# Kernel optimization log

Hardware: AMD Instinct MI355X
Metric: run time of the kernel (lower is better)

## Reference

```python
import jax, jax.numpy as jnp
import numpy as np

DIM = 512
HEADS = 8
AGENT = 49
POOL = 7  # int(sqrt(49))
EPS = 1e-5  # BatchNorm eps


def _adaptive_avg_pool(x, out_hw):
    # torch AdaptiveAvgPool2d semantics: bin i covers [floor(i*H/out), ceil((i+1)*H/out))
    B, C, H, W = x.shape
    cs = jnp.cumsum(jnp.cumsum(x, axis=2), axis=3)
    cs = jnp.pad(cs, ((0, 0), (0, 0), (1, 0), (1, 0)))  # integral image, [B,C,H+1,W+1]
    hs = np.floor(np.arange(out_hw) * H / out_hw).astype(np.int32)
    he = np.ceil((np.arange(out_hw) + 1) * H / out_hw).astype(np.int32)
    ws = np.floor(np.arange(out_hw) * W / out_hw).astype(np.int32)
    we = np.ceil((np.arange(out_hw) + 1) * W / out_hw).astype(np.int32)
    area = ((he - hs)[:, None] * (we - ws)[None, :]).astype(np.float32)
    s = (cs[:, :, he][:, :, :, we] - cs[:, :, hs][:, :, :, we]
         - cs[:, :, he][:, :, :, ws] + cs[:, :, hs][:, :, :, ws])
    return s / area


def setup_inputs() -> dict:
    key = jax.random.key(0)
    ks = jax.random.split(key, 8)
    d = DIM

    def w(k, shape, s=0.02):
        return jax.random.normal(k, shape, jnp.float32) * s

    return {
        "x": jax.random.normal(ks[0], (16, d, 32, 32), jnp.float32),
        "H": 32,
        "W": 32,
        "q_w": w(ks[1], (d, d)),
        "kv_w": w(ks[2], (2 * d, d)),
        "dw_w": w(ks[3], (d, 1, 3, 3), 0.1),   # depthwise 3x3, groups=d
        "dw_b": jnp.zeros((d,), jnp.float32),
        "bn_gamma": jnp.ones((d,), jnp.float32),
        "bn_beta": jnp.zeros((d,), jnp.float32),
        "bn_mean": jnp.zeros((d,), jnp.float32),
        "bn_var": jnp.ones((d,), jnp.float32),
        "pw_w": w(ks[4], (d, d, 1, 1)),          # pointwise 1x1 conv
        "pw_b": jnp.zeros((d,), jnp.float32),
        "proj_w": w(ks[5], (d, d)),
        "proj_b": jnp.zeros((d,), jnp.float32),
        "enh1_w": w(ks[6], (d, d)),
        "enh1_b": jnp.zeros((d,), jnp.float32),
        "enh2_w": w(ks[7], (d, d)),
        "enh2_b": jnp.zeros((d,), jnp.float32),
    }


def reference(x, H, W, q_w, kv_w, dw_w, dw_b, bn_gamma, bn_beta, bn_mean, bn_var,
              pw_w, pw_b, proj_w, proj_b, enh1_w, enh1_b, enh2_w, enh2_b):
    B, C, H, W = x.shape  # torch re-reads sizes from x
    N = H * W
    hd = C // HEADS
    scale = hd ** -0.5
    dn = ('NCHW', 'OIHW', 'NCHW')

    x_flat = x.reshape(B, C, N).transpose(0, 2, 1)            # [B,N,C]
    q = (x_flat @ q_w.T).reshape(B, N, HEADS, hd).transpose(0, 2, 1, 3)  # [B,h,N,hd]
    kv = (x_flat @ kv_w.T).reshape(B, N, 2, HEADS, hd).transpose(2, 0, 3, 1, 4)
    k, v = kv[0], kv[1]                                        # [B,h,N,hd]

    # agent tokens (faithful raw reshapes as in the torch code)
    a = _adaptive_avg_pool(x, POOL)                            # [B,C,7,7]
    a = a.reshape(B, C, AGENT).transpose(0, 2, 1)              # [B,49,C]
    a = a.reshape(B, C, POOL, POOL)                            # raw reshape (torch bug, kept)
    a = jax.lax.conv_general_dilated(a, dw_w, (1, 1), 'SAME',
                                     feature_group_count=C, dimension_numbers=dn)
    a = a + dw_b[None, :, None, None]
    a = (a - bn_mean[None, :, None, None]) * jax.lax.rsqrt(bn_var + EPS)[None, :, None, None]
    a = a * bn_gamma[None, :, None, None] + bn_beta[None, :, None, None]
    a = jax.nn.relu(a)
    a = jax.lax.conv_general_dilated(a, pw_w, (1, 1), 'SAME', dimension_numbers=dn)
    a = a + pw_b[None, :, None, None]
    a = a.reshape(B, AGENT, C)                                 # raw reshape
    a = a.reshape(B, HEADS, AGENT, hd)                         # raw reshape (torch bug, kept)

    # stage 1: agent <- kv
    agent_attn = jax.nn.softmax(jnp.einsum('bhad,bhnd->bhan', a, k) * scale, axis=-1)
    agg = jnp.einsum('bhan,bhnd->bhad', agent_attn, v)         # [B,h,49,hd]
    # stage 2: q <- agent
    q_attn = jax.nn.softmax(jnp.einsum('bhnd,bhad->bhna', q, a) * scale, axis=-1)
    enh = jnp.einsum('bhna,bhad->bhnd', q_attn, agg)           # [B,h,N,hd]
    enh = enh.transpose(0, 2, 1, 3).reshape(B, N, C)

    x_out = enh @ proj_w.T + proj_b
    out = (jax.nn.relu(x_out @ enh1_w.T + enh1_b) @ enh2_w.T + enh2_b) + x_out
    return out.reshape(B, C, H, W)  # raw reshape as in torch
```

## Files before the change

kernel.cpp:

```cpp
#include <hip/hip_runtime.h>
#include <stdint.h>


typedef float f32x4 __attribute__((ext_vector_type(4)));
typedef short s16x8 __attribute__((ext_vector_type(8)));

typedef __attribute__((address_space(1))) void glob_v;
typedef __attribute__((address_space(3))) void lds_v;
#define GLD16(g, l) \
  __builtin_amdgcn_global_load_lds((glob_v*)(g), (lds_v*)(l), 16, 0, 0)

__device__ __forceinline__ float bf2f(unsigned short u) {
  union { unsigned int i; float f; } v; v.i = ((unsigned int)u) << 16; return v.f;
}
__device__ __forceinline__ unsigned short f2bf(float f) {
  union { float f; unsigned int i; } v; v.f = f;
  return (unsigned short)((v.i + 0x7FFFu + ((v.i >> 16) & 1u)) >> 16);
}

__constant__ int ws7[7] = {0, 4, 9, 13, 18, 22, 27};
__constant__ int we7[7] = {5, 10, 14, 19, 23, 28, 32};

__global__ __launch_bounds__(256) void k_transpose(const float* __restrict__ x,
                                                   unsigned short* __restrict__ xT,
                                                   float* __restrict__ p_rows) {
  __shared__ float tile[64][65];
  const int b = blockIdx.z, c0 = blockIdx.y * 64, n0 = blockIdx.x * 64;
  const int t = threadIdx.x, tn = t & 63, tg = t >> 6;
#pragma unroll
  for (int i = 0; i < 16; ++i) {
    const int c_l = tg * 16 + i;
    tile[c_l][tn] = x[(b * 512 + c0 + c_l) * 1024 + n0 + tn];
  }
  __syncthreads();
#pragma unroll
  for (int i = 0; i < 16; ++i) {
    const int n_l = tg * 16 + i;
    xT[(b * 1024 + n0 + n_l) * 512 + c0 + tn] = f2bf(tile[tn][n_l]);
  }
  if (t < 128) {
    const int c_l = t >> 1, rw = t & 1;
    const int rowg = blockIdx.x * 2 + rw;
    const float* src = &tile[c_l][rw * 32];
    float* dst = p_rows + ((b * 512 + c0 + c_l) * 32 + rowg) * 8;
#pragma unroll
    for (int jb = 0; jb < 7; ++jb) {
      float s = 0.f;
      for (int cc = ws7[jb]; cc < we7[jb]; ++cc) s += src[cc];
      dst[jb] = s;
    }
  }
}

__global__ __launch_bounds__(256) void k_poolred(const float* __restrict__ p_rows,
                                                 float* __restrict__ p) {
  const int u = blockIdx.x * 256 + threadIdx.x;
  if (u >= 401408) return;
  const int bc = u / 49, ij = u % 49;
  const int i = ij / 7, j = ij % 7;
  float s = 0.f;
  for (int r = ws7[i]; r < we7[i]; ++r) s += p_rows[bc * 256 + r * 8 + j];
  const float area = (float)((we7[i] - ws7[i]) * (we7[j] - ws7[j]));
  p[u] = s / area;
}

__global__ __launch_bounds__(256) void k_weights(
    const float* __restrict__ qw, const float* __restrict__ kvw,
    const float* __restrict__ pjw, const float* __restrict__ w1,
    const float* __restrict__ w2, unsigned short* __restrict__ Wqkv,
    unsigned short* __restrict__ Wpj, unsigned short* __restrict__ W1,
    unsigned short* __restrict__ W2) {
  const int u = blockIdx.x * 256 + threadIdx.x;
  const float* s; unsigned short* d; int su, du;
  if (u < 196608) { d = Wqkv; du = u;
    if (u < 65536) { s = qw; su = u; } else { s = kvw; su = u - 65536; } }
  else if (u < 262144) { s = pjw; su = u - 196608; d = Wpj; du = su; }
  else if (u < 327680) { s = w1; su = u - 262144; d = W1; du = su; }
  else { s = w2; su = u - 327680; d = W2; du = su; }
  const f32x4 val = ((const f32x4*)s)[su];
  uint2 pk;
  pk.x = (unsigned)f2bf(val[0]) | ((unsigned)f2bf(val[1]) << 16);
  pk.y = (unsigned)f2bf(val[2]) | ((unsigned)f2bf(val[3]) << 16);
  ((uint2*)d)[du] = pk;
}

__global__ __launch_bounds__(256) void k_dw(
    const float* __restrict__ p, const float* __restrict__ dww,
    const float* __restrict__ dwb, const float* __restrict__ g,
    const float* __restrict__ be, const float* __restrict__ mean,
    const float* __restrict__ var, float* __restrict__ r) {
  const int t = threadIdx.x, s = t & 63;
  if (s >= 49) return;
  const int bc = blockIdx.x * 4 + (t >> 6);
  const int b = bc >> 9, c = bc & 511;
  const int i = s / 7, j = s % 7;
  float sum = 0.f;
#pragma unroll
  for (int ki = 0; ki < 3; ++ki)
#pragma unroll
    for (int kj = 0; kj < 3; ++kj) {
      const int ii = i + ki - 1, jj = j + kj - 1;
      if (ii < 0 || ii > 6 || jj < 0 || jj > 6) continue;
      const int f = c * 49 + ii * 7 + jj;
      sum += dww[c * 9 + ki * 3 + kj] * p[(b * 512 + (f & 511)) * 49 + (f >> 9)];
    }
  sum += dwb[c];
  sum = (sum - mean[c]) * rsqrtf(var[c] + 1e-5f) * g[c] + be[c];
  r[bc * 49 + s] = fmaxf(sum, 0.f);
}

__global__ __launch_bounds__(256) void k_pw(const float* __restrict__ r,
                                            const float* __restrict__ w,
                                            const float* __restrict__ bias,
                                            float* __restrict__ A) {
  __shared__ float wl[128 * 36];
  __shared__ float rl[128 * 64];
  const int blk = blockIdx.x;
  const int b = blk >> 4, cg = blk & 15;
  const int t = threadIdx.x, wv = t >> 6, lane = t & 63;
  float acc[8];
#pragma unroll
  for (int j = 0; j < 8; ++j) acc[j] = 0.f;
  for (int ch = 0; ch < 4; ++ch) {
    __syncthreads();
#pragma unroll
    for (int u = t; u < 4096; u += 256) {
      const int co = u >> 7, ci = u & 127;
      wl[ci * 36 + co] = w[(cg * 32 + co) * 512 + ch * 128 + ci];
    }
    for (int u = t; u < 6272; u += 256) {
      const int ci = u / 49, s = u % 49;
      rl[ci * 64 + s] = r[b * 25088 + ch * 6272 + u];
    }
    __syncthreads();
#pragma unroll 4
    for (int ci = 0; ci < 128; ++ci) {
      const f32x4 w0 = *(const f32x4*)(wl + ci * 36 + wv * 8);
      const f32x4 w1 = *(const f32x4*)(wl + ci * 36 + wv * 8 + 4);
      const float rv = rl[ci * 64 + lane];
#pragma unroll
      for (int j = 0; j < 4; ++j) { acc[j] += w0[j] * rv; acc[4 + j] += w1[j] * rv; }
    }
  }
  if (lane < 49) {
#pragma unroll
    for (int j = 0; j < 8; ++j) {
      const int co = cg * 32 + wv * 8 + j;
      A[b * 25088 + co * 49 + lane] = acc[j] + bias[co];
    }
  }
}

template <int MODE>
__global__ __launch_bounds__(256) void k_gemm(
    const unsigned short* __restrict__ A, const unsigned short* __restrict__ B,
    unsigned short* __restrict__ oq, unsigned short* __restrict__ ok,
    unsigned short* __restrict__ ov, float* __restrict__ of,
    unsigned short* __restrict__ obf, const float* __restrict__ bias,
    const float* __restrict__ resid, float* __restrict__ dout) {
  __shared__ unsigned short As[2][4096];
  __shared__ unsigned short Bs[2][4096];
  const int t = threadIdx.x;
  constexpr int NB = (MODE == 0) ? 12 : 4;
  constexpr int NWG = NB * 128;
  const int swz = ((int)blockIdx.x & 7) * (NWG >> 3) + ((int)blockIdx.x >> 3);
  const int n0 = (swz % NB) * 128, m0 = (swz / NB) * 128;
  const int w = t >> 6, lane = t & 63;
  const int wr = w >> 1, wc = w & 1, lr = lane & 15, lg = lane >> 4;
  const int row = t >> 2, q = t & 3;
  const unsigned short* gA = A + m0 * 512;
  const unsigned short* gB = B + n0 * 512;

  auto stage = [&](int cur, int kt) {
    const unsigned short* sa = gA + row * 512 + kt * 32 + q * 8;
    const unsigned short* sb = gB + row * 512 + kt * 32 + q * 8;
    unsigned short* da = As[cur] + w * 512;
    unsigned short* db = Bs[cur] + w * 512;
    GLD16(sa, da);
    GLD16(sa + 32768, da + 2048);
    GLD16(sb, db);
    GLD16(sb + 32768, db + 2048);
  };

  f32x4 acc[4][4];
#pragma unroll
  for (int mi = 0; mi < 4; ++mi)
#pragma unroll
    for (int ni = 0; ni < 4; ++ni)
#pragma unroll
      for (int rr = 0; rr < 4; ++rr) acc[mi][ni][rr] = 0.f;

  stage(0, 0);
  __syncthreads();
  int cur = 0;
  for (int kt = 0; kt < 16; ++kt) {
    if (kt < 15) stage(cur ^ 1, kt + 1);
    const unsigned short* Ac = As[cur];
    const unsigned short* Bc = Bs[cur];
    s16x8 af[4], bfr[4];
#pragma unroll
    for (int mi = 0; mi < 4; ++mi)
      af[mi] = *(const s16x8*)(Ac + (wr * 64 + mi * 16 + lr) * 32 + lg * 8);
#pragma unroll
    for (int ni = 0; ni < 4; ++ni)
      bfr[ni] = *(const s16x8*)(Bc + (wc * 64 + ni * 16 + lr) * 32 + lg * 8);
#pragma unroll
    for (int mi = 0; mi < 4; ++mi)
#pragma unroll
      for (int ni = 0; ni < 4; ++ni)
        acc[mi][ni] = __builtin_amdgcn_mfma_f32_16x16x32_bf16(af[mi], bfr[ni],
                                                              acc[mi][ni], 0, 0, 0);
    __syncthreads();
    cur ^= 1;
  }

#pragma unroll
  for (int mi = 0; mi < 4; ++mi)
#pragma unroll
    for (int ni = 0; ni < 4; ++ni)
#pragma unroll
      for (int rr = 0; rr < 4; ++rr) {
        const int gm = m0 + wr * 64 + mi * 16 + lg * 4 + rr;
        const int gn = n0 + wc * 64 + ni * 16 + lr;
        const float val = acc[mi][ni][rr];
        if (MODE == 0) {
          const int b = gm >> 10, n = gm & 1023;
          const int hh = (gn >> 6) & 7, dd = gn & 63;
          const int idx = ((b * 8 + hh) * 1024 + n) * 64 + dd;
          const unsigned short bv = f2bf(val);
          if (gn < 512) oq[idx] = bv;
          else if (gn < 1024) ok[idx] = bv;
          else ov[idx] = bv;
        } else if (MODE == 1) {
          const float v2 = val + bias[gn];
          of[gm * 512 + gn] = v2;
          obf[gm * 512 + gn] = f2bf(v2);
        } else if (MODE == 2) {
          const float v2 = fmaxf(val + bias[gn], 0.f);
          obf[gm * 512 + gn] = f2bf(v2);
        } else {
          dout[gm * 512 + gn] = val + bias[gn] + resid[gm * 512 + gn];
        }
      }
}

__global__ __launch_bounds__(256) void k_aflash(
    const float* __restrict__ Abuf, const unsigned short* __restrict__ kbf,
    const unsigned short* __restrict__ vbf, float* __restrict__ numT,
    float* __restrict__ denG) {
  __shared__ unsigned short A_lds[64 * 72];
  __shared__ unsigned short K_lds[64 * 72];
  __shared__ unsigned short VT_lds[64 * 72];
  __shared__ unsigned short P_lds[64 * 72];
  const int blk = blockIdx.x;
  const int bh = blk >> 1, half = blk & 1;
  const int b = bh >> 3, h = bh & 7;
  const int t = threadIdx.x, w = t >> 6, lane = t & 63;
  const int lr = lane & 15, lg = lane >> 4;

  for (int u = t; u < 64 * 72; u += 256) A_lds[u] = 0;
  __syncthreads();
  for (int u = t; u < 3136; u += 256) {
    const int d = u / 49, ag = u % 49;
    A_lds[ag * 72 + d] = f2bf(Abuf[b * 25088 + (h * 64 + d) * 49 + ag]);
  }

  const unsigned short* kbase = kbf + bh * 65536 + half * 512 * 64;
  const unsigned short* vbase = vbf + bh * 65536 + half * 512 * 64;

  f32x4 num[4];
#pragma unroll
  for (int ni = 0; ni < 4; ++ni)
#pragma unroll
    for (int rr = 0; rr < 4; ++rr) num[ni][rr] = 0.f;
  float den[4] = {0.f, 0.f, 0.f, 0.f};

  for (int c = 0; c < 8; ++c) {
    const int n0 = c * 64;
    __syncthreads();
#pragma unroll
    for (int u = t; u < 512; u += 256) {
      const int rw = u >> 3, qq = u & 7;
      *(s16x8*)(K_lds + rw * 72 + qq * 8) =
          *(const s16x8*)(kbase + (n0 + rw) * 64 + qq * 8);
    }
#pragma unroll
    for (int u = t; u < 512; u += 256) {
      const int n_l = u & 63, qq = u >> 6;
      const s16x8 v = *(const s16x8*)(vbase + (n0 + n_l) * 64 + qq * 8);
#pragma unroll
      for (int j = 0; j < 8; ++j)
        VT_lds[(qq * 8 + j) * 72 + n_l] = (unsigned short)v[j];
    }
    __syncthreads();
    f32x4 s[4];
#pragma unroll
    for (int ni = 0; ni < 4; ++ni)
#pragma unroll
      for (int rr = 0; rr < 4; ++rr) s[ni][rr] = 0.f;
#pragma unroll
    for (int kk = 0; kk < 2; ++kk) {
      const s16x8 afr = *(const s16x8*)(A_lds + (w * 16 + lr) * 72 + kk * 32 + lg * 8);
#pragma unroll
      for (int ni = 0; ni < 4; ++ni) {
        const s16x8 bfr =
            *(const s16x8*)(K_lds + (ni * 16 + lr) * 72 + kk * 32 + lg * 8);
        s[ni] = __builtin_amdgcn_mfma_f32_16x16x32_bf16(afr, bfr, s[ni], 0, 0, 0);
      }
    }
#pragma unroll
    for (int ni = 0; ni < 4; ++ni)
#pragma unroll
      for (int rr = 0; rr < 4; ++rr) {
        const float p = __expf(s[ni][rr] * 0.125f);
        den[rr] += p;
        P_lds[(w * 16 + lg * 4 + rr) * 72 + ni * 16 + lr] = f2bf(p);
      }
#pragma unroll
    for (int kk = 0; kk < 2; ++kk) {
      const s16x8 pa = *(const s16x8*)(P_lds + (w * 16 + lr) * 72 + kk * 32 + lg * 8);
#pragma unroll
      for (int ni = 0; ni < 4; ++ni) {
        const s16x8 vfr =
            *(const s16x8*)(VT_lds + (ni * 16 + lr) * 72 + kk * 32 + lg * 8);
        num[ni] = __builtin_amdgcn_mfma_f32_16x16x32_bf16(pa, vfr, num[ni], 0, 0, 0);
      }
    }
  }
#pragma unroll
  for (int rr = 0; rr < 4; ++rr) {
#pragma unroll
    for (int o = 1; o < 16; o <<= 1) den[rr] += __shfl_xor(den[rr], o, 64);
  }
  const int obase = (half * 128 + bh) * 4096;
#pragma unroll
  for (int ni = 0; ni < 4; ++ni)
    *(f32x4*)(numT + obase + (ni * 16 + lr) * 64 + w * 16 + lg * 4) = num[ni];
  if (lr == 0) {
    f32x4 dv;
#pragma unroll
    for (int rr = 0; rr < 4; ++rr) dv[rr] = den[rr];
    *(f32x4*)(denG + (half * 128 + bh) * 64 + w * 16 + lg * 4) = dv;
  }
}

__global__ __launch_bounds__(256) void k_attn2(
    const float* __restrict__ Abuf, const float* __restrict__ numT,
    const float* __restrict__ denG, const unsigned short* __restrict__ qbf,
    unsigned short* __restrict__ enh) {
  __shared__ unsigned short A_lds[64 * 72];
  __shared__ unsigned short G_lds[64 * 72];
  __shared__ unsigned short P2_lds[4][64 * 72];
  __shared__ float den_lds[64];
  const int blk = blockIdx.x;
  const int bh = blk >> 2, nq = blk & 3;
  const int b = bh >> 3, h = bh & 7;
  const int t = threadIdx.x, w = t >> 6, lane = t & 63;
  const int lr = lane & 15, lg = lane >> 4;

  if (t < 64) den_lds[t] = 1.f / (denG[bh * 64 + t] + denG[8192 + bh * 64 + t]);
  for (int u = t; u < 64 * 72; u += 256) A_lds[u] = 0;
  __syncthreads();
  for (int u = t; u < 3136; u += 256) {
    const int d = u / 49, ag = u % 49;
    A_lds[ag * 72 + d] = f2bf(Abuf[b * 25088 + (h * 64 + d) * 49 + ag]);
  }
  for (int u = t; u < 4096; u += 256) {
    const int d = u >> 6, ag = u & 63;
    const float v = (numT[bh * 4096 + u] + numT[524288 + bh * 4096 + u]) * den_lds[ag];
    G_lds[d * 72 + ag] = f2bf(v);
  }
  __syncthreads();

  const int nbase = nq * 256 + w * 64;
  const unsigned short* qp = qbf + (bh * 1024 + nbase) * 64;
  s16x8 qf[4][2];
#pragma unroll
  for (int mi = 0; mi < 4; ++mi)
#pragma unroll
    for (int kk = 0; kk < 2; ++kk)
      qf[mi][kk] = *(const s16x8*)(qp + (mi * 16 + lr) * 64 + kk * 32 + lg * 8);

  f32x4 L[4][4];
#pragma unroll
  for (int mi = 0; mi < 4; ++mi)
#pragma unroll
    for (int ni = 0; ni < 4; ++ni)
#pragma unroll
      for (int rr = 0; rr < 4; ++rr) L[mi][ni][rr] = 0.f;
#pragma unroll
  for (int kk = 0; kk < 2; ++kk)
#pragma unroll
    for (int ni = 0; ni < 4; ++ni) {
      const s16x8 bfr = *(const s16x8*)(A_lds + (ni * 16 + lr) * 72 + kk * 32 + lg * 8);
#pragma unroll
      for (int mi = 0; mi < 4; ++mi)
        L[mi][ni] = __builtin_amdgcn_mfma_f32_16x16x32_bf16(qf[mi][kk], bfr,
                                                            L[mi][ni], 0, 0, 0);
    }
  unsigned short* pw = P2_lds[w];
#pragma unroll
  for (int mi = 0; mi < 4; ++mi) {
    float ps[4][4];
    float rs[4];
#pragma unroll
    for (int rr = 0; rr < 4; ++rr) rs[rr] = 0.f;
#pragma unroll
    for (int ni = 0; ni < 4; ++ni) {
      const bool valid = (ni < 3) | (lr == 0);
#pragma unroll
      for (int rr = 0; rr < 4; ++rr) {
        const float p = valid ? __expf(L[mi][ni][rr] * 0.125f) : 0.f;
        ps[ni][rr] = p;
        rs[rr] += p;
      }
    }
#pragma unroll
    for (int rr = 0; rr < 4; ++rr) {
#pragma unroll
      for (int o = 1; o < 16; o <<= 1) rs[rr] += __shfl_xor(rs[rr], o, 64);
      rs[rr] = 1.f / rs[rr];
    }
#pragma unroll
    for (int ni = 0; ni < 4; ++ni)
#pragma unroll
      for (int rr = 0; rr < 4; ++rr)
        pw[(mi * 16 + lg * 4 + rr) * 72 + ni * 16 + lr] = f2bf(ps[ni][rr] * rs[rr]);
  }
#pragma unroll
  for (int mi = 0; mi < 4; ++mi) {
    f32x4 e[4];
#pragma unroll
    for (int ni = 0; ni < 4; ++ni)
#pragma unroll
      for (int rr = 0; rr < 4; ++rr) e[ni][rr] = 0.f;
#pragma unroll
    for (int kk = 0; kk < 2; ++kk) {
      const s16x8 pa = *(const s16x8*)(pw + (mi * 16 + lr) * 72 + kk * 32 + lg * 8);
#pragma unroll
      for (int ni = 0; ni < 4; ++ni) {
        const s16x8 gb = *(const s16x8*)(G_lds + (ni * 16 + lr) * 72 + kk * 32 + lg * 8);
        e[ni] = __builtin_amdgcn_mfma_f32_16x16x32_bf16(pa, gb, e[ni], 0, 0, 0);
      }
    }
#pragma unroll
    for (int ni = 0; ni < 4; ++ni)
#pragma unroll
      for (int rr = 0; rr < 4; ++rr) {
        const int n = nbase + mi * 16 + lg * 4 + rr;
        enh[(b * 1024 + n) * 512 + h * 64 + ni * 16 + lr] = f2bf(e[ni][rr]);
      }
  }
}

extern "C" void kernel_launch(void* const* d_in, const int* in_sizes, int n_in,
                              void* d_out, int out_size, void* d_ws, size_t ws_size,
                              hipStream_t stream) {
  const float* x    = (const float*)d_in[0];
  const float* q_w  = (const float*)d_in[3];
  const float* kv_w = (const float*)d_in[4];
  const float* dw_w = (const float*)d_in[5];
  const float* dw_b = (const float*)d_in[6];
  const float* bn_g = (const float*)d_in[7];
  const float* bn_b = (const float*)d_in[8];
  const float* bn_m = (const float*)d_in[9];
  const float* bn_v = (const float*)d_in[10];
  const float* pw_w = (const float*)d_in[11];
  const float* pw_b = (const float*)d_in[12];
  const float* pj_w = (const float*)d_in[13];
  const float* pj_b = (const float*)d_in[14];
  const float* e1_w = (const float*)d_in[15];
  const float* e1_b = (const float*)d_in[16];
  const float* e2_w = (const float*)d_in[17];
  const float* e2_b = (const float*)d_in[18];

  char* base = (char*)d_ws;
  size_t off = 0;
  auto alloc = [&](size_t bytes) -> void* {
    void* r = base + off;
    off += (bytes + 255) & ~(size_t)255;
    return r;
  };
  unsigned short* Wqkv = (unsigned short*)alloc(786432ull * 2);
  unsigned short* Wpj  = (unsigned short*)alloc(262144ull * 2);
  unsigned short* W1   = (unsigned short*)alloc(262144ull * 2);
  unsigned short* W2   = (unsigned short*)alloc(262144ull * 2);
  unsigned short* xT   = (unsigned short*)alloc(8388608ull * 2);
  unsigned short* qb   = (unsigned short*)alloc(8388608ull * 2);
  unsigned short* kb   = (unsigned short*)alloc(8388608ull * 2);
  unsigned short* vb   = (unsigned short*)alloc(8388608ull * 2);
  float* prow = (float*)alloc(2097152ull * 4);
  float* pbuf = (float*)alloc(401408ull * 4);
  float* rbuf = (float*)alloc(401408ull * 4);
  float* Abuf = (float*)alloc(401408ull * 4);
  float* numT = (float*)alloc(1048576ull * 4);
  float* denG = (float*)alloc(16384ull * 4);
  unsigned short* enh  = (unsigned short*)alloc(8388608ull * 2);
  float* xout = (float*)alloc(8388608ull * 4);
  unsigned short* xoutb = (unsigned short*)alloc(8388608ull * 2);
  unsigned short* h1    = (unsigned short*)alloc(8388608ull * 2);
  (void)ws_size; (void)in_sizes; (void)n_in; (void)out_size;

  k_weights<<<1536, 256, 0, stream>>>(q_w, kv_w, pj_w, e1_w, e2_w, Wqkv, Wpj, W1, W2);
  k_transpose<<<dim3(16, 8, 16), 256, 0, stream>>>(x, xT, prow);
  k_poolred<<<1568, 256, 0, stream>>>(prow, pbuf);
  k_dw<<<2048, 256, 0, stream>>>(pbuf, dw_w, dw_b, bn_g, bn_b, bn_m, bn_v, rbuf);
  k_pw<<<256, 256, 0, stream>>>(rbuf, pw_w, pw_b, Abuf);
  k_gemm<0><<<1536, 256, 0, stream>>>(xT, Wqkv, qb, kb, vb,
                                      nullptr, nullptr, nullptr, nullptr, nullptr);
  k_aflash<<<256, 256, 0, stream>>>(Abuf, kb, vb, numT, denG);
  k_attn2<<<512, 256, 0, stream>>>(Abuf, numT, denG, qb, enh);
  k_gemm<1><<<512, 256, 0, stream>>>(enh, Wpj, nullptr, nullptr, nullptr,
                                     xout, xoutb, pj_b, nullptr, nullptr);
  k_gemm<2><<<512, 256, 0, stream>>>(xoutb, W1, nullptr, nullptr, nullptr,
                                     nullptr, h1, e1_b, nullptr, nullptr);
  k_gemm<3><<<512, 256, 0, stream>>>(h1, W2, nullptr, nullptr, nullptr,
                                     nullptr, nullptr, e2_b, xout, (float*)d_out);
}
```

Before: 211.0 us.

## Swizzle GEMM LDS layout and split agent attention into quarters

```diff
diff --git a/kernel.cpp b/kernel.cpp
--- a/kernel.cpp
+++ b/kernel.cpp
@@ -167,19 +167,24 @@
   const int n0 = (swz % NB) * 128, m0 = (swz / NB) * 128;
   const int w = t >> 6, lane = t & 63;
   const int wr = w >> 1, wc = w & 1, lr = lane & 15, lg = lane >> 4;
-  const int row = t >> 2, q = t & 3;
   const unsigned short* gA = A + m0 * 512;
   const unsigned short* gB = B + n0 * 512;
 
+  const int s_rp = t >> 3;
+  const int s_g = (t & 7) ^ (s_rp & 7);
+  const int s_r = (s_rp << 1) | (s_g >> 2);
+  const int s_kq = (s_g & 3) * 8;
   auto stage = [&](int cur, int kt) {
-    const unsigned short* sa = gA + row * 512 + kt * 32 + q * 8;
-    const unsigned short* sb = gB + row * 512 + kt * 32 + q * 8;
-    unsigned short* da = As[cur] + w * 512;
-    unsigned short* db = Bs[cur] + w * 512;
-    GLD16(sa, da);
-    GLD16(sa + 32768, da + 2048);
-    GLD16(sb, db);
-    GLD16(sb + 32768, db + 2048);
+    const int ko = kt * 32 + s_kq;
+    GLD16(gA + s_r * 512 + ko, As[cur] + w * 512);
+    GLD16(gA + (s_r + 64) * 512 + ko, As[cur] + 2048 + w * 512);
+    GLD16(gB + s_r * 512 + ko, Bs[cur] + w * 512);
+    GLD16(gB + (s_r + 64) * 512 + ko, Bs[cur] + 2048 + w * 512);
+  };
+  auto ldsw = [&](const unsigned short* hb, int rl, int lgq) -> s16x8 {
+    const int rp = rl >> 1;
+    const int gs = (((rl & 1) << 2) | lgq) ^ (rp & 7);
+    return *(const s16x8*)(hb + rp * 64 + gs * 8);
   };
 
   f32x4 acc[4][4];
@@ -195,15 +200,13 @@
   int cur = 0;
   for (int kt = 0; kt < 16; ++kt) {
     if (kt < 15) stage(cur ^ 1, kt + 1);
-    const unsigned short* Ac = As[cur];
-    const unsigned short* Bc = Bs[cur];
+    const unsigned short* Ah = As[cur] + wr * 2048;
+    const unsigned short* Bh = Bs[cur] + wc * 2048;
     s16x8 af[4], bfr[4];
 #pragma unroll
-    for (int mi = 0; mi < 4; ++mi)
-      af[mi] = *(const s16x8*)(Ac + (wr * 64 + mi * 16 + lr) * 32 + lg * 8);
-#pragma unroll
-    for (int ni = 0; ni < 4; ++ni)
-      bfr[ni] = *(const s16x8*)(Bc + (wc * 64 + ni * 16 + lr) * 32 + lg * 8);
+    for (int mi = 0; mi < 4; ++mi) af[mi] = ldsw(Ah, mi * 16 + lr, lg);
+#pragma unroll
+    for (int ni = 0; ni < 4; ++ni) bfr[ni] = ldsw(Bh, ni * 16 + lr, lg);
 #pragma unroll
     for (int mi = 0; mi < 4; ++mi)
 #pragma unroll
@@ -253,7 +256,7 @@
   __shared__ unsigned short VT_lds[64 * 72];
   __shared__ unsigned short P_lds[64 * 72];
   const int blk = blockIdx.x;
-  const int bh = blk >> 1, half = blk & 1;
+  const int bh = blk >> 2, qtr = blk & 3;
   const int b = bh >> 3, h = bh & 7;
   const int t = threadIdx.x, w = t >> 6, lane = t & 63;
   const int lr = lane & 15, lg = lane >> 4;
@@ -265,8 +268,8 @@
     A_lds[ag * 72 + d] = f2bf(Abuf[b * 25088 + (h * 64 + d) * 49 + ag]);
   }
 
-  const unsigned short* kbase = kbf + bh * 65536 + half * 512 * 64;
-  const unsigned short* vbase = vbf + bh * 65536 + half * 512 * 64;
+  const unsigned short* kbase = kbf + bh * 65536 + qtr * 256 * 64;
+  const unsigned short* vbase = vbf + bh * 65536 + qtr * 256 * 64;
 
   f32x4 num[4];
 #pragma unroll
@@ -275,7 +278,7 @@
     for (int rr = 0; rr < 4; ++rr) num[ni][rr] = 0.f;
   float den[4] = {0.f, 0.f, 0.f, 0.f};
 
-  for (int c = 0; c < 8; ++c) {
+  for (int c = 0; c < 4; ++c) {
     const int n0 = c * 64;
     __syncthreads();
 #pragma unroll
@@ -332,7 +335,7 @@
 #pragma unroll
     for (int o = 1; o < 16; o <<= 1) den[rr] += __shfl_xor(den[rr], o, 64);
   }
-  const int obase = (half * 128 + bh) * 4096;
+  const int obase = (qtr * 128 + bh) * 4096;
 #pragma unroll
   for (int ni = 0; ni < 4; ++ni)
     *(f32x4*)(numT + obase + (ni * 16 + lr) * 64 + w * 16 + lg * 4) = num[ni];
@@ -340,7 +343,7 @@
     f32x4 dv;
 #pragma unroll
     for (int rr = 0; rr < 4; ++rr) dv[rr] = den[rr];
-    *(f32x4*)(denG + (half * 128 + bh) * 64 + w * 16 + lg * 4) = dv;
+    *(f32x4*)(denG + (qtr * 128 + bh) * 64 + w * 16 + lg * 4) = dv;
   }
 }
 
@@ -358,7 +361,9 @@
   const int t = threadIdx.x, w = t >> 6, lane = t & 63;
   const int lr = lane & 15, lg = lane >> 4;
 
-  if (t < 64) den_lds[t] = 1.f / (denG[bh * 64 + t] + denG[8192 + bh * 64 + t]);
+  if (t < 64)
+    den_lds[t] = 1.f / (denG[bh * 64 + t] + denG[8192 + bh * 64 + t] +
+                        denG[16384 + bh * 64 + t] + denG[24576 + bh * 64 + t]);
   for (int u = t; u < 64 * 72; u += 256) A_lds[u] = 0;
   __syncthreads();
   for (int u = t; u < 3136; u += 256) {
@@ -367,7 +372,9 @@
   }
   for (int u = t; u < 4096; u += 256) {
     const int d = u >> 6, ag = u & 63;
-    const float v = (numT[bh * 4096 + u] + numT[524288 + bh * 4096 + u]) * den_lds[ag];
+    const float v = (numT[bh * 4096 + u] + numT[524288 + bh * 4096 + u] +
+                     numT[1048576 + bh * 4096 + u] + numT[1572864 + bh * 4096 + u]) *
+                    den_lds[ag];
     G_lds[d * 72 + ag] = f2bf(v);
   }
   __syncthreads();
@@ -493,8 +500,8 @@
   float* pbuf = (float*)alloc(401408ull * 4);
   float* rbuf = (float*)alloc(401408ull * 4);
   float* Abuf = (float*)alloc(401408ull * 4);
-  float* numT = (float*)alloc(1048576ull * 4);
-  float* denG = (float*)alloc(16384ull * 4);
+  float* numT = (float*)alloc(2097152ull * 4);
+  float* denG = (float*)alloc(32768ull * 4);
   unsigned short* enh  = (unsigned short*)alloc(8388608ull * 2);
   float* xout = (float*)alloc(8388608ull * 4);
   unsigned short* xoutb = (unsigned short*)alloc(8388608ull * 2);
@@ -508,7 +515,7 @@
   k_pw<<<256, 256, 0, stream>>>(rbuf, pw_w, pw_b, Abuf);
   k_gemm<0><<<1536, 256, 0, stream>>>(xT, Wqkv, qb, kb, vb,
                                       nullptr, nullptr, nullptr, nullptr, nullptr);
-  k_aflash<<<256, 256, 0, stream>>>(Abuf, kb, vb, numT, denG);
+  k_aflash<<<512, 256, 0, stream>>>(Abuf, kb, vb, numT, denG);
   k_attn2<<<512, 256, 0, stream>>>(Abuf, numT, denG, qb, enh);
   k_gemm<1><<<512, 256, 0, stream>>>(enh, Wpj, nullptr, nullptr, nullptr,
                                      xout, xoutb, pj_b, nullptr, nullptr);
```

Result: faster. 206.8 us (-2.0%).
